# Optimization experiments

Measured on AMD Instinct MI355X. Metric: run time of the kernel, lower is better.

The kernel has to match this reference:

```python
import jax, jax.numpy as jnp
import numpy as np

EMBED = 1024
HEADS = 16
HEAD_DIM = EMBED // HEADS


def setup_inputs() -> dict:
    key = jax.random.key(0)
    ks = jax.random.split(key, 11)
    B, S, D = 2, 2048, EMBED
    scale = 1.0 / np.sqrt(D)
    inp = {
        "q": jax.random.normal(ks[0], (B, S, D), jnp.float32),
        "k": jax.random.normal(ks[1], (B, S, D), jnp.float32),
        "v": jax.random.normal(ks[2], (B, S, D), jnp.float32),
        "Wq": jax.random.normal(ks[3], (D, D), jnp.float32) * scale,
        "bq": jnp.zeros((D,), jnp.float32),
        "Wk": jax.random.normal(ks[4], (D, D), jnp.float32) * scale,
        "bk": jnp.zeros((D,), jnp.float32),
        "Wv": jax.random.normal(ks[5], (D, D), jnp.float32) * scale,
        "bv": jnp.zeros((D,), jnp.float32),
        "Wo": jax.random.normal(ks[6], (D, D), jnp.float32) * scale,
        "bo": jnp.zeros((D,), jnp.float32),
    }
    return inp


def _split_heads(x):
    b, n, c = x.shape
    return x.reshape(b, n, HEADS, c // HEADS).transpose(0, 2, 1, 3)  # [b,h,n,dh]


def reference(q, k, v, Wq, bq, Wk, bk, Wv, bv, Wo, bo):
    qh = _split_heads(q @ Wq + bq)
    kh = _split_heads(k @ Wk + bk)
    vh = _split_heads(v @ Wv + bv)
    scale = 1.0 / jnp.sqrt(jnp.asarray(HEAD_DIM, qh.dtype))
    att = jnp.einsum("bhqd,bhkd->bhqk", qh, kh) * scale
    att = jax.nn.softmax(att, axis=-1)
    out = jnp.einsum("bhqk,bhkd->bhqd", att, vh)
    b, h, n, dh = out.shape
    out = out.transpose(0, 2, 1, 3).reshape(b, n, h * dh)
    return out @ Wo + bo
```

## Files before the change

### kernel.cpp

```cpp
#include <hip/hip_runtime.h>
#include <hip/hip_bf16.h>
#include <stdint.h>

typedef unsigned short u16;
typedef __bf16 bf16x8 __attribute__((ext_vector_type(8)));
typedef float f32x4 __attribute__((ext_vector_type(4)));
typedef unsigned int u32x4 __attribute__((ext_vector_type(4)));
typedef unsigned int u32x2 __attribute__((ext_vector_type(2)));

#define S_LEN 2048
#define DMODEL 1024
#define NHEAD 16
#define DHEAD 64
#define MROWS 4096

__device__ __forceinline__ u16 f2b(float f) {
  __hip_bfloat16 h = __float2bfloat16(f);
  union { __hip_bfloat16 h; u16 u; } c;
  c.h = h;
  return c.u;
}
__device__ __forceinline__ unsigned int pk2(float lo, float hi) {
  return (unsigned int)f2b(lo) | ((unsigned int)f2b(hi) << 16);
}

__device__ __forceinline__ void gload16(const void* g, void* l) {
  __builtin_amdgcn_global_load_lds(
      (const __attribute__((address_space(1))) unsigned int*)(uintptr_t)g,
      (__attribute__((address_space(3))) unsigned int*)(uintptr_t)l,
      16, 0, 0);
}

__global__ __launch_bounds__(256) void prep(
    const float* __restrict__ q, const float* __restrict__ k, const float* __restrict__ v,
    const float* __restrict__ Wq, const float* __restrict__ Wk,
    const float* __restrict__ Wv, const float* __restrict__ Wo,
    u16* __restrict__ Qx, u16* __restrict__ Kx, u16* __restrict__ Vx,
    u16* __restrict__ Wqt, u16* __restrict__ Wkt,
    u16* __restrict__ Wvt, u16* __restrict__ Wot) {
  __shared__ u16 tile[64][65];
  const int z = blockIdx.z;
  const int tid = threadIdx.x;
  if (z < 3) {
    const float* src = (z == 0) ? q : (z == 1) ? k : v;
    u16* dst = (z == 0) ? Qx : (z == 1) ? Kx : Vx;
    const size_t i8 = ((size_t)blockIdx.x * 256 + tid) * 8;
    float4 a = *(const float4*)(src + i8);
    float4 b = *(const float4*)(src + i8 + 4);
    u16 o[8];
    o[0] = f2b(a.x); o[1] = f2b(a.y); o[2] = f2b(a.z); o[3] = f2b(a.w);
    o[4] = f2b(b.x); o[5] = f2b(b.y); o[6] = f2b(b.z); o[7] = f2b(b.w);
    *(u32x4*)(dst + i8) = *(const u32x4*)o;
    return;
  }
  if (blockIdx.x >= 256) return;
  const int zz = z - 3;
  const float* W = (zz == 0) ? Wq : (zz == 1) ? Wk : (zz == 2) ? Wv : Wo;
  u16* Wt = (zz == 0) ? Wqt : (zz == 1) ? Wkt : (zz == 2) ? Wvt : Wot;
  const int n0 = (blockIdx.x & 15) * 64, k0 = (blockIdx.x >> 4) * 64;
#pragma unroll
  for (int j = 0; j < 16; j++) {
    int idx = j * 256 + tid;
    int r = idx >> 6, c = idx & 63;
    tile[r][c] = f2b(W[(size_t)(k0 + r) * DMODEL + n0 + c]);
  }
  __syncthreads();
#pragma unroll
  for (int j = 0; j < 16; j++) {
    int idx = j * 256 + tid;
    int r = idx >> 6, c = idx & 63;
    Wt[(size_t)(n0 + r) * DMODEL + k0 + c] = tile[c][r];
  }
}

template <int MODE>
__device__ __forceinline__ void gemm_body(const u16* __restrict__ A,
                                          const u16* __restrict__ Bt,
                                          const float* __restrict__ bias,
                                          void* __restrict__ Cv) {
  constexpr int K = DMODEL;
  __shared__ u16 As[128 * 32];
  __shared__ u16 Bs[128 * 32];
  const int tid = threadIdx.x;
  const int wave = tid >> 6, lane = tid & 63;
  const int quad = lane >> 4, l15 = lane & 15;
  const int wr = wave >> 1, wc = wave & 1;
  const int brow = blockIdx.y, bcol = blockIdx.x;

  f32x4 acc[4][4] = {};

  for (int k0 = 0; k0 < K; k0 += 32) {
    __syncthreads();
#pragma unroll
    for (int t = 0; t < 2; t++) {
      const int slot = t * 256 + wave * 64 + lane;
      const int row = slot >> 2;
      const int col = (slot & 3) << 3;
      const int ldsb = (t * 256 + wave * 64) * 8;
      gload16(A + (size_t)(brow * 128 + row) * K + k0 + col, As + ldsb);
      gload16(Bt + (size_t)(bcol * 128 + row) * K + k0 + col, Bs + ldsb);
    }
    __syncthreads();

    bf16x8 af[4], bfm[4];
#pragma unroll
    for (int i = 0; i < 4; i++)
      af[i] = *(const bf16x8*)(As + (wr * 64 + i * 16 + l15) * 32 + quad * 8);
#pragma unroll
    for (int j = 0; j < 4; j++)
      bfm[j] = *(const bf16x8*)(Bs + (wc * 64 + j * 16 + l15) * 32 + quad * 8);
#pragma unroll
    for (int i = 0; i < 4; i++)
#pragma unroll
      for (int j = 0; j < 4; j++)
        acc[i][j] = __builtin_amdgcn_mfma_f32_16x16x32_bf16(af[i], bfm[j], acc[i][j], 0, 0, 0);
  }

#pragma unroll
  for (int i = 0; i < 4; i++)
#pragma unroll
    for (int j = 0; j < 4; j++) {
      const int col = bcol * 128 + wc * 64 + j * 16 + l15;
      const float bv = bias[col];
      if (MODE == 2) {
        const int srow = brow * 128 + wr * 64 + i * 16 + quad * 4;
        const int bb = srow >> 11, s = srow & (S_LEN - 1);
        u32x2 pd;
        pd.x = pk2(acc[i][j][0] + bv, acc[i][j][1] + bv);
        pd.y = pk2(acc[i][j][2] + bv, acc[i][j][3] + bv);
        *(u32x2*)((u16*)Cv + ((size_t)(bb * 1024 + col)) * S_LEN + s) = pd;
      } else {
#pragma unroll
        for (int r = 0; r < 4; r++) {
          const int row = brow * 128 + wr * 64 + i * 16 + quad * 4 + r;
          if (MODE == 1)
            ((float*)Cv)[(size_t)row * DMODEL + col] = acc[i][j][r] + bv;
          else
            ((u16*)Cv)[(size_t)row * DMODEL + col] = f2b(acc[i][j][r] + bv);
        }
      }
    }
}

__global__ __launch_bounds__(256) void gemm_qkv(
    const u16* __restrict__ Qx, const u16* __restrict__ Kx, const u16* __restrict__ Vx,
    const u16* __restrict__ Wqt, const u16* __restrict__ Wkt, const u16* __restrict__ Wvt,
    const float* __restrict__ bq, const float* __restrict__ bk, const float* __restrict__ bv,
    u16* __restrict__ Qp, u16* __restrict__ Kp, u16* __restrict__ Vt) {
  const int z = blockIdx.z;
  if (z == 2) {
    gemm_body<2>(Vx, Wvt, bv, Vt);
  } else {
    const u16* A = (z == 0) ? Qx : Kx;
    const u16* Bt = (z == 0) ? Wqt : Wkt;
    const float* bias = (z == 0) ? bq : bk;
    u16* C = (z == 0) ? Qp : Kp;
    gemm_body<0>(A, Bt, bias, C);
  }
}

__global__ __launch_bounds__(256) void gemm_out(
    const u16* __restrict__ A, const u16* __restrict__ Bt,
    const float* __restrict__ bias, float* __restrict__ C) {
  gemm_body<1>(A, Bt, bias, C);
}

#define EXP2SCALE 0.180336880112f
__global__ __launch_bounds__(256) void attn(const u16* __restrict__ Qp,
                                            const u16* __restrict__ Kp,
                                            const u16* __restrict__ Vt,
                                            u16* __restrict__ Op) {
  __shared__ u16 Ks[64 * 72];
  __shared__ u16 Vs[64 * 72];
  __shared__ u16 Ps[128 * 72];

  const int tid = threadIdx.x;
  const int wave = tid >> 6, lane = tid & 63;
  const int quad = lane >> 4, l15 = lane & 15;
  const int b = blockIdx.z, h = blockIdx.y, s0 = blockIdx.x * 128;

  const size_t baseK = ((size_t)(b * S_LEN)) * DMODEL + h * DHEAD;
  const size_t baseV = ((size_t)((b * NHEAD + h) * DHEAD)) * S_LEN;

  bf16x8 b1;
  {
    union { u16 a[8]; bf16x8 v; } c;
    u16 one = (l15 == 0) ? 0x3F80 : 0;
#pragma unroll
    for (int j = 0; j < 8; j++) c.a[j] = one;
    b1 = c.v;
  }

  bf16x8 qf[2][2];
#pragma unroll
  for (int rb = 0; rb < 2; rb++)
#pragma unroll
    for (int kx = 0; kx < 2; kx++)
      qf[rb][kx] = *(const bf16x8*)(Qp +
          ((size_t)(b * S_LEN + s0 + wave * 32 + rb * 16 + l15)) * DMODEL +
          h * DHEAD + kx * 32 + quad * 8);

  f32x4 oacc[2][4] = {};
  f32x4 lacc[2] = {};

  for (int kt = 0; kt < 32; kt++) {
    u32x4 kreg[2], vreg[2];
#pragma unroll
    for (int t = 0; t < 2; t++) {
      int idx = t * 256 + tid;
      int r = idx >> 3, c = (idx & 7) * 8;
      kreg[t] = *(const u32x4*)(Kp + baseK + (size_t)(kt * 64 + r) * DMODEL + c);
      vreg[t] = *(const u32x4*)(Vt + baseV + (size_t)r * S_LEN + kt * 64 + c);
    }
    __syncthreads();
#pragma unroll
    for (int t = 0; t < 2; t++) {
      int idx = t * 256 + tid;
      int r = idx >> 3, c = (idx & 7) * 8;
      *(u32x4*)(Ks + r * 72 + c) = kreg[t];
      *(u32x4*)(Vs + r * 72 + c) = vreg[t];
    }
    __syncthreads();

    f32x4 sfT[2][4] = {};
#pragma unroll
    for (int n = 0; n < 4; n++) {
#pragma unroll
      for (int kx = 0; kx < 2; kx++) {
        bf16x8 ka = *(const bf16x8*)(Ks + (n * 16 + l15) * 72 + kx * 32 + quad * 8);
        sfT[0][n] = __builtin_amdgcn_mfma_f32_16x16x32_bf16(ka, qf[0][kx], sfT[0][n], 0, 0, 0);
        sfT[1][n] = __builtin_amdgcn_mfma_f32_16x16x32_bf16(ka, qf[1][kx], sfT[1][n], 0, 0, 0);
      }
    }

#pragma unroll
    for (int rb = 0; rb < 2; rb++)
#pragma unroll
      for (int n = 0; n < 4; n++) {
        float p0 = __builtin_amdgcn_exp2f(sfT[rb][n][0] * EXP2SCALE);
        float p1 = __builtin_amdgcn_exp2f(sfT[rb][n][1] * EXP2SCALE);
        float p2 = __builtin_amdgcn_exp2f(sfT[rb][n][2] * EXP2SCALE);
        float p3 = __builtin_amdgcn_exp2f(sfT[rb][n][3] * EXP2SCALE);
        u32x2 pd;
        pd.x = pk2(p0, p1);
        pd.y = pk2(p2, p3);
        *(u32x2*)(Ps + (wave * 32 + rb * 16 + l15) * 72 + n * 16 + quad * 4) = pd;
      }

#pragma unroll
    for (int kx = 0; kx < 2; kx++) {
      bf16x8 ap0 = *(const bf16x8*)(Ps + (wave * 32 + l15) * 72 + kx * 32 + quad * 8);
      bf16x8 ap1 = *(const bf16x8*)(Ps + (wave * 32 + 16 + l15) * 72 + kx * 32 + quad * 8);
      lacc[0] = __builtin_amdgcn_mfma_f32_16x16x32_bf16(ap0, b1, lacc[0], 0, 0, 0);
      lacc[1] = __builtin_amdgcn_mfma_f32_16x16x32_bf16(ap1, b1, lacc[1], 0, 0, 0);
#pragma unroll
      for (int n = 0; n < 4; n++) {
        bf16x8 bv = *(const bf16x8*)(Vs + (n * 16 + l15) * 72 + kx * 32 + quad * 8);
        oacc[0][n] = __builtin_amdgcn_mfma_f32_16x16x32_bf16(ap0, bv, oacc[0][n], 0, 0, 0);
        oacc[1][n] = __builtin_amdgcn_mfma_f32_16x16x32_bf16(ap1, bv, oacc[1][n], 0, 0, 0);
      }
    }
  }

#pragma unroll
  for (int rb = 0; rb < 2; rb++) {
    float inv[4];
#pragma unroll
    for (int r = 0; r < 4; r++)
      inv[r] = 1.0f / __shfl(lacc[rb][r], quad * 16);
#pragma unroll
    for (int n = 0; n < 4; n++)
#pragma unroll
      for (int r = 0; r < 4; r++) {
        int row = s0 + wave * 32 + rb * 16 + quad * 4 + r;
        int col = h * DHEAD + n * 16 + l15;
        Op[((size_t)(b * S_LEN + row)) * DMODEL + col] = f2b(oacc[rb][n][r] * inv[r]);
      }
  }
}

extern "C" void kernel_launch(void* const* d_in, const int* in_sizes, int n_in,
                              void* d_out, int out_size, void* d_ws, size_t ws_size,
                              hipStream_t stream) {
  const float* q  = (const float*)d_in[0];
  const float* k  = (const float*)d_in[1];
  const float* v  = (const float*)d_in[2];
  const float* Wq = (const float*)d_in[3];
  const float* bq = (const float*)d_in[4];
  const float* Wk = (const float*)d_in[5];
  const float* bk = (const float*)d_in[6];
  const float* Wv = (const float*)d_in[7];
  const float* bv = (const float*)d_in[8];
  const float* Wo = (const float*)d_in[9];
  const float* bo = (const float*)d_in[10];

  char* w = (char*)d_ws;
  const size_t WSZ = (size_t)DMODEL * DMODEL * 2;
  const size_t XSZ = (size_t)MROWS * DMODEL * 2;
  u16* Wqt = (u16*)(w);
  u16* Wkt = (u16*)(w + WSZ);
  u16* Wvt = (u16*)(w + 2 * WSZ);
  u16* Wot = (u16*)(w + 3 * WSZ);
  u16* Qx  = (u16*)(w + 4 * WSZ);
  u16* Kx  = (u16*)(w + 4 * WSZ + XSZ);
  u16* Vx  = (u16*)(w + 4 * WSZ + 2 * XSZ);
  u16* Qp  = (u16*)(w + 4 * WSZ + 3 * XSZ);
  u16* Kp  = (u16*)(w + 4 * WSZ + 4 * XSZ);
  u16* Vt  = (u16*)(w + 4 * WSZ + 5 * XSZ);
  u16* Op  = (u16*)(w + 4 * WSZ + 6 * XSZ);

  prep<<<dim3(2048, 1, 7), 256, 0, stream>>>(q, k, v, Wq, Wk, Wv, Wo,
                                             Qx, Kx, Vx, Wqt, Wkt, Wvt, Wot);
  gemm_qkv<<<dim3(8, 32, 3), 256, 0, stream>>>(Qx, Kx, Vx, Wqt, Wkt, Wvt,
                                               bq, bk, bv, Qp, Kp, Vt);
  attn<<<dim3(16, 16, 2), 256, 0, stream>>>(Qp, Kp, Vt, Op);
  gemm_out<<<dim3(8, 32, 1), 256, 0, stream>>>(Op, Wot, bo, (float*)d_out);
}
```

Before: 237.9 us.

## Halve attention query tile, prefetch next K/V tile, swizzle LDS, set MFMA priority

The attention kernel now processes 64 query rows per block instead of 128, doubling the grid to 1024 blocks for more parallelism on the GPU. K/V tiles for the next iteration are loaded into registers while the current tile is computed, so global loads overlap with math. Padded LDS rows are replaced by an XOR swizzle to avoid bank conflicts, and s_setprio is raised around the MFMA sections. The trade-off is less K/V reuse per block: each K/V tile is loaded twice as many times overall.

```diff
diff --git a/kernel.cpp b/kernel.cpp
--- a/kernel.cpp
+++ b/kernel.cpp
@@ -170,14 +170,14 @@
                                             const u16* __restrict__ Kp,
                                             const u16* __restrict__ Vt,
                                             u16* __restrict__ Op) {
-  __shared__ u16 Ks[64 * 72];
-  __shared__ u16 Vs[64 * 72];
-  __shared__ u16 Ps[128 * 72];
+  __shared__ u16 Ks[64 * 64];
+  __shared__ u16 Vs[64 * 64];
+  __shared__ u16 Ps[64 * 64];
 
   const int tid = threadIdx.x;
   const int wave = tid >> 6, lane = tid & 63;
   const int quad = lane >> 4, l15 = lane & 15;
-  const int b = blockIdx.z, h = blockIdx.y, s0 = blockIdx.x * 128;
+  const int b = blockIdx.z, h = blockIdx.y, s0 = blockIdx.x * 64;
 
   const size_t baseK = ((size_t)(b * S_LEN)) * DMODEL + h * DHEAD;
   const size_t baseV = ((size_t)((b * NHEAD + h) * DHEAD)) * S_LEN;
@@ -191,92 +191,102 @@
     b1 = c.v;
   }
 
-  bf16x8 qf[2][2];
-#pragma unroll
-  for (int rb = 0; rb < 2; rb++)
-#pragma unroll
-    for (int kx = 0; kx < 2; kx++)
-      qf[rb][kx] = *(const bf16x8*)(Qp +
-          ((size_t)(b * S_LEN + s0 + wave * 32 + rb * 16 + l15)) * DMODEL +
-          h * DHEAD + kx * 32 + quad * 8);
-
-  f32x4 oacc[2][4] = {};
-  f32x4 lacc[2] = {};
+  bf16x8 qf[2];
+#pragma unroll
+  for (int kx = 0; kx < 2; kx++)
+    qf[kx] = *(const bf16x8*)(Qp +
+        ((size_t)(b * S_LEN + s0 + wave * 16 + l15)) * DMODEL +
+        h * DHEAD + kx * 32 + quad * 8);
+
+  f32x4 oacc[4] = {};
+  f32x4 lacc = {};
+
+  u32x4 kreg[2], vreg[2];
+#pragma unroll
+  for (int t = 0; t < 2; t++) {
+    int idx = t * 256 + tid;
+    int r = idx >> 3, c = (idx & 7) * 8;
+    kreg[t] = *(const u32x4*)(Kp + baseK + (size_t)r * DMODEL + c);
+    vreg[t] = *(const u32x4*)(Vt + baseV + (size_t)r * S_LEN + c);
+  }
 
   for (int kt = 0; kt < 32; kt++) {
-    u32x4 kreg[2], vreg[2];
+    __syncthreads();
 #pragma unroll
     for (int t = 0; t < 2; t++) {
       int idx = t * 256 + tid;
       int r = idx >> 3, c = (idx & 7) * 8;
-      kreg[t] = *(const u32x4*)(Kp + baseK + (size_t)(kt * 64 + r) * DMODEL + c);
-      vreg[t] = *(const u32x4*)(Vt + baseV + (size_t)r * S_LEN + kt * 64 + c);
+      int di = (r * 64 + c) ^ ((r & 7) << 3);
+      *(u32x4*)(Ks + di) = kreg[t];
+      *(u32x4*)(Vs + di) = vreg[t];
     }
     __syncthreads();
-#pragma unroll
-    for (int t = 0; t < 2; t++) {
-      int idx = t * 256 + tid;
-      int r = idx >> 3, c = (idx & 7) * 8;
-      *(u32x4*)(Ks + r * 72 + c) = kreg[t];
-      *(u32x4*)(Vs + r * 72 + c) = vreg[t];
-    }
-    __syncthreads();
-
-    f32x4 sfT[2][4] = {};
+
+    if (kt < 31) {
+#pragma unroll
+      for (int t = 0; t < 2; t++) {
+        int idx = t * 256 + tid;
+        int r = idx >> 3, c = (idx & 7) * 8;
+        kreg[t] = *(const u32x4*)(Kp + baseK + (size_t)((kt + 1) * 64 + r) * DMODEL + c);
+        vreg[t] = *(const u32x4*)(Vt + baseV + (size_t)r * S_LEN + (kt + 1) * 64 + c);
+      }
+    }
+
+    f32x4 sfT[4] = {};
+    __builtin_amdgcn_s_setprio(1);
 #pragma unroll
     for (int n = 0; n < 4; n++) {
 #pragma unroll
       for (int kx = 0; kx < 2; kx++) {
-        bf16x8 ka = *(const bf16x8*)(Ks + (n * 16 + l15) * 72 + kx * 32 + quad * 8);
-        sfT[0][n] = __builtin_amdgcn_mfma_f32_16x16x32_bf16(ka, qf[0][kx], sfT[0][n], 0, 0, 0);
-        sfT[1][n] = __builtin_amdgcn_mfma_f32_16x16x32_bf16(ka, qf[1][kx], sfT[1][n], 0, 0, 0);
+        bf16x8 ka = *(const bf16x8*)(Ks +
+            ((((n * 16 + l15) * 64) + kx * 32 + quad * 8) ^ ((l15 & 7) << 3)));
+        sfT[n] = __builtin_amdgcn_mfma_f32_16x16x32_bf16(ka, qf[kx], sfT[n], 0, 0, 0);
       }
     }
-
-#pragma unroll
-    for (int rb = 0; rb < 2; rb++)
+    __builtin_amdgcn_s_setprio(0);
+
+#pragma unroll
+    for (int n = 0; n < 4; n++) {
+      float p0 = __builtin_amdgcn_exp2f(sfT[n][0] * EXP2SCALE);
+      float p1 = __builtin_amdgcn_exp2f(sfT[n][1] * EXP2SCALE);
+      float p2 = __builtin_amdgcn_exp2f(sfT[n][2] * EXP2SCALE);
+      float p3 = __builtin_amdgcn_exp2f(sfT[n][3] * EXP2SCALE);
+      u32x2 pd;
+      pd.x = pk2(p0, p1);
+      pd.y = pk2(p2, p3);
+      int row = wave * 16 + l15;
+      *(u32x2*)(Ps + ((row * 64 + n * 16 + quad * 4) ^ ((row & 7) << 3))) = pd;
+    }
+
+    __builtin_amdgcn_s_setprio(1);
+#pragma unroll
+    for (int kx = 0; kx < 2; kx++) {
+      int prow = wave * 16 + l15;
+      bf16x8 ap = *(const bf16x8*)(Ps +
+          ((prow * 64 + kx * 32 + quad * 8) ^ ((prow & 7) << 3)));
+      lacc = __builtin_amdgcn_mfma_f32_16x16x32_bf16(ap, b1, lacc, 0, 0, 0);
 #pragma unroll
       for (int n = 0; n < 4; n++) {
-        float p0 = __builtin_amdgcn_exp2f(sfT[rb][n][0] * EXP2SCALE);
-        float p1 = __builtin_amdgcn_exp2f(sfT[rb][n][1] * EXP2SCALE);
-        float p2 = __builtin_amdgcn_exp2f(sfT[rb][n][2] * EXP2SCALE);
-        float p3 = __builtin_amdgcn_exp2f(sfT[rb][n][3] * EXP2SCALE);
-        u32x2 pd;
-        pd.x = pk2(p0, p1);
-        pd.y = pk2(p2, p3);
-        *(u32x2*)(Ps + (wave * 32 + rb * 16 + l15) * 72 + n * 16 + quad * 4) = pd;
+        bf16x8 bv = *(const bf16x8*)(Vs +
+            ((((n * 16 + l15) * 64) + kx * 32 + quad * 8) ^ ((l15 & 7) << 3)));
+        oacc[n] = __builtin_amdgcn_mfma_f32_16x16x32_bf16(ap, bv, oacc[n], 0, 0, 0);
       }
-
-#pragma unroll
-    for (int kx = 0; kx < 2; kx++) {
-      bf16x8 ap0 = *(const bf16x8*)(Ps + (wave * 32 + l15) * 72 + kx * 32 + quad * 8);
-      bf16x8 ap1 = *(const bf16x8*)(Ps + (wave * 32 + 16 + l15) * 72 + kx * 32 + quad * 8);
-      lacc[0] = __builtin_amdgcn_mfma_f32_16x16x32_bf16(ap0, b1, lacc[0], 0, 0, 0);
-      lacc[1] = __builtin_amdgcn_mfma_f32_16x16x32_bf16(ap1, b1, lacc[1], 0, 0, 0);
-#pragma unroll
-      for (int n = 0; n < 4; n++) {
-        bf16x8 bv = *(const bf16x8*)(Vs + (n * 16 + l15) * 72 + kx * 32 + quad * 8);
-        oacc[0][n] = __builtin_amdgcn_mfma_f32_16x16x32_bf16(ap0, bv, oacc[0][n], 0, 0, 0);
-        oacc[1][n] = __builtin_amdgcn_mfma_f32_16x16x32_bf16(ap1, bv, oacc[1][n], 0, 0, 0);
-      }
-    }
-  }
-
-#pragma unroll
-  for (int rb = 0; rb < 2; rb++) {
-    float inv[4];
-#pragma unroll
-    for (int r = 0; r < 4; r++)
-      inv[r] = 1.0f / __shfl(lacc[rb][r], quad * 16);
-#pragma unroll
-    for (int n = 0; n < 4; n++)
-#pragma unroll
-      for (int r = 0; r < 4; r++) {
-        int row = s0 + wave * 32 + rb * 16 + quad * 4 + r;
-        int col = h * DHEAD + n * 16 + l15;
-        Op[((size_t)(b * S_LEN + row)) * DMODEL + col] = f2b(oacc[rb][n][r] * inv[r]);
-      }
-  }
+    }
+    __builtin_amdgcn_s_setprio(0);
+  }
+
+  float inv[4];
+#pragma unroll
+  for (int r = 0; r < 4; r++)
+    inv[r] = 1.0f / __shfl(lacc[r], quad * 16);
+#pragma unroll
+  for (int n = 0; n < 4; n++)
+#pragma unroll
+    for (int r = 0; r < 4; r++) {
+      int row = s0 + wave * 16 + quad * 4 + r;
+      int col = h * DHEAD + n * 16 + l15;
+      Op[((size_t)(b * S_LEN + row)) * DMODEL + col] = f2b(oacc[n][r] * inv[r]);
+    }
 }
 
 extern "C" void kernel_launch(void* const* d_in, const int* in_sizes, int n_in,
@@ -313,6 +323,6 @@
                                              Qx, Kx, Vx, Wqt, Wkt, Wvt, Wot);
   gemm_qkv<<<dim3(8, 32, 3), 256, 0, stream>>>(Qx, Kx, Vx, Wqt, Wkt, Wvt,
                                                bq, bk, bv, Qp, Kp, Vt);
-  attn<<<dim3(16, 16, 2), 256, 0, stream>>>(Qp, Kp, Vt, Op);
+  attn<<<dim3(32, 16, 2), 256, 0, stream>>>(Qp, Kp, Vt, Op);
   gemm_out<<<dim3(8, 32, 1), 256, 0, stream>>>(Op, Wot, bo, (float*)d_out);
 }
```

Result: no change. 241.1 us (+1.3%).
